# Kernel tuning notes

Measured on AMD Instinct MI355X. Metric: run time of the kernel, lower is better.

The kernel has to match this reference:

```python
import jax, jax.numpy as jnp
import numpy as np

N_NODES = 50000
N_EDGES = 800000
D = 128
NEG_SLOPE = 0.01
LN_EPS = 1e-5


def gcn_conv(x, W, b, src, dst, n_nodes):
    # Linear transform: [N, D_in] @ [D_in, D_out]
    h = x @ W
    # Symmetric degree normalization (self-loops already included in src/dst)
    deg = jax.ops.segment_sum(jnp.ones_like(dst, dtype=h.dtype), dst, num_segments=n_nodes)
    dinv = jnp.where(deg > 0, jax.lax.rsqrt(deg), 0.0)
    coef = dinv[src] * dinv[dst]                      # [E]
    msg = h[src] * coef[:, None]                      # gather + scale, [E, D]
    out = jax.ops.segment_sum(msg, dst, num_segments=n_nodes)  # scatter-add
    return out + b


def layer_norm(x, gamma, beta):
    mu = jnp.mean(x, axis=-1, keepdims=True)
    var = jnp.mean(jnp.square(x - mu), axis=-1, keepdims=True)
    return (x - mu) * jax.lax.rsqrt(var + LN_EPS) * gamma + beta


def setup_inputs() -> dict:
    key = jax.random.key(0)
    ks = jax.random.split(key, 8)
    x = jax.random.normal(ks[0], (N_NODES, D), dtype=jnp.float32)
    edge_index = jax.random.randint(ks[1], (2, N_EDGES), 0, N_NODES, dtype=jnp.int64)
    s = 1.0 / np.sqrt(D)
    W1 = jax.random.uniform(ks[2], (D, D), jnp.float32, -s, s)
    b1 = jnp.zeros((D,), jnp.float32)
    W2 = jax.random.uniform(ks[3], (D, D), jnp.float32, -s, s)
    b2 = jnp.zeros((D,), jnp.float32)
    ln1_g = jnp.ones((D,), jnp.float32)
    ln1_b = jnp.zeros((D,), jnp.float32)
    ln2_g = jnp.ones((D,), jnp.float32)
    ln2_b = jnp.zeros((D,), jnp.float32)
    return {"x": x, "edge_index": edge_index, "W1": W1, "b1": b1,
            "ln1_g": ln1_g, "ln1_b": ln1_b, "W2": W2, "b2": b2,
            "ln2_g": ln2_g, "ln2_b": ln2_b}


def reference(x, edge_index, W1, b1, ln1_g, ln1_b, W2, b2, ln2_g, ln2_b):
    n = x.shape[0]
    # add self-loops (PyG GCNConv default)
    loops = jnp.arange(n, dtype=edge_index.dtype)
    src = jnp.concatenate([edge_index[0], loops])
    dst = jnp.concatenate([edge_index[1], loops])

    residual = x
    h = gcn_conv(x, W1, b1, src, dst, n)
    h = jax.nn.leaky_relu(h, NEG_SLOPE)
    h = layer_norm(h + residual, ln1_g, ln1_b)
    h = gcn_conv(h, W2, b2, src, dst, n)
    return jax.nn.leaky_relu(layer_norm(h + residual, ln2_g, ln2_b), NEG_SLOPE)
```

## Files before the change

### kernel.cpp

```cpp
#include <hip/hip_runtime.h>
#include <hip/hip_bf16.h>

#define NN 50000
#define NE 800000
#define D 128
#define NEG_SLOPE 0.01f
#define LN_EPS 1e-5f

#define NPB 256
#define NB 196
#define CAP 6144
#define ECH 8192
#define NCH ((NE + ECH - 1) / ECH)
#define NDEG 256
#define NGEMM ((NN + 63) / 64)

typedef __attribute__((ext_vector_type(8))) short bf16x8;
typedef __attribute__((ext_vector_type(4))) float f32x4;
typedef __attribute__((ext_vector_type(4))) int i32x4;

__device__ inline unsigned short f2bf(float f) {
    unsigned u = __float_as_uint(f);
    unsigned r = 0x7FFFu + ((u >> 16) & 1u);
    return (unsigned short)((u + r) >> 16);
}
__device__ inline void bf2x(unsigned u, float& lo, float& hi) {
    lo = __uint_as_float(u << 16);
    hi = __uint_as_float(u & 0xFFFF0000u);
}


struct BucketLDS {
    int hist[NB], lcur[NB], gbase[NB];
    int tmp[256];
};
struct GemmLDS {
    unsigned short a[64 * 128];
};
union FusedLDS { BucketLDS b; GemmLDS g; };

__device__ inline void gemm_body(GemmLDS& L, const float* __restrict__ A,
                                 const unsigned short* __restrict__ WT,
                                 unsigned short* __restrict__ out, int m0, int n, int t) {
    #pragma unroll
    for (int it = 0; it < 4; ++it) {
        int idx = it * 256 + t;
        int row = idx >> 4, c = idx & 15;
        int grow = m0 + row;
        uint4 w = make_uint4(0u, 0u, 0u, 0u);
        if (grow < n) {
            float4 v0 = *(const float4*)&A[(size_t)grow * D + c * 8];
            float4 v1 = *(const float4*)&A[(size_t)grow * D + c * 8 + 4];
            w.x = (unsigned)f2bf(v0.x) | ((unsigned)f2bf(v0.y) << 16);
            w.y = (unsigned)f2bf(v0.z) | ((unsigned)f2bf(v0.w) << 16);
            w.z = (unsigned)f2bf(v1.x) | ((unsigned)f2bf(v1.y) << 16);
            w.w = (unsigned)f2bf(v1.z) | ((unsigned)f2bf(v1.w) << 16);
        }
        int byte = (row * 256 + c * 16) ^ ((row & 7) << 4);
        *(uint4*)((char*)L.a + byte) = w;
    }
    __syncthreads();

    int wv = t >> 6, l = t & 63;
    int lrow = l & 15, lgrp = l >> 4;
    int arow = wv * 16 + lrow;

    f32x4 acc[8];
    #pragma unroll
    for (int nf = 0; nf < 8; ++nf) acc[nf] = (f32x4){0.f, 0.f, 0.f, 0.f};

    #pragma unroll
    for (int kk = 0; kk < 4; ++kk) {
        int abyte = (arow * 256 + kk * 64 + lgrp * 16) ^ ((arow & 7) << 4);
        bf16x8 afrag = *(bf16x8*)((char*)L.a + abyte);
        #pragma unroll
        for (int nf = 0; nf < 8; ++nf) {
            int bcol = nf * 16 + lrow;
            bf16x8 bfrag = *(const bf16x8*)&WT[bcol * 128 + kk * 32 + lgrp * 8];
            acc[nf] = __builtin_amdgcn_mfma_f32_16x16x32_bf16(afrag, bfrag, acc[nf], 0, 0, 0);
        }
    }

    #pragma unroll
    for (int nf = 0; nf < 8; ++nf) {
        #pragma unroll
        for (int r = 0; r < 4; ++r) {
            int grow = m0 + wv * 16 + lgrp * 4 + r;
            if (grow < n) out[(size_t)grow * D + nf * 16 + lrow] = f2bf(acc[nf][r]);
        }
    }
}

__global__ __launch_bounds__(256) void fused1(const int* __restrict__ src,
                                              const int* __restrict__ dst,
                                              int* __restrict__ bcursor,
                                              int2* __restrict__ bedge,
                                              int* __restrict__ deg,
                                              const float* __restrict__ x,
                                              const unsigned short* __restrict__ wt1,
                                              unsigned short* __restrict__ hbf) {
    __shared__ FusedLDS u;
    int bid = blockIdx.x, t = threadIdx.x;

    if (bid < NCH) {
        BucketLDS& L = u.b;
        int e0 = bid * ECH;
        int ecnt = min(ECH, NE - e0);
        if (t < NB) L.hist[t] = 0;
        __syncthreads();
        for (int k = t; k < ecnt; k += 256) atomicAdd(&L.hist[dst[e0 + k] >> 8], 1);
        __syncthreads();
        if (t < NB) {
            L.gbase[t] = atomicAdd(&bcursor[t], L.hist[t]);
            L.lcur[t] = 0;
        }
        __syncthreads();
        for (int k = t; k < ecnt; k += 256) {
            int s = src[e0 + k], d = dst[e0 + k];
            int b = d >> 8;
            int p = atomicAdd(&L.lcur[b], 1);
            bedge[(size_t)b * CAP + L.gbase[b] + p] = make_int2(s, d);
        }
    } else if (bid < NCH + NDEG) {
        for (int k = (bid - NCH) * 256 + t; k < NE; k += NDEG * 256)
            atomicAdd(&deg[dst[k]], 1);
    } else {
        gemm_body(u.g, x, wt1, hbf, (bid - NCH - NDEG) * 64, NN, t);
    }
}

__global__ __launch_bounds__(256) void fused2(const int2* __restrict__ bedge,
                                              const int* __restrict__ bcnt,
                                              const int* __restrict__ deg,
                                              float* __restrict__ dinv,
                                              int2* __restrict__ rowinfo,
                                              int* __restrict__ ticket,
                                              int2* __restrict__ csr_pair) {
    __shared__ int tmp[256];
    __shared__ int rl[NPB], cur[NPB];
    __shared__ float sdinv[NPB];
    __shared__ int base;
    int b = blockIdx.x, t = threadIdx.x;
    int node = b * NPB + t;
    int dg = (node < NN) ? deg[node] : 0;
    float dv = rsqrtf((float)(dg + 1));
    sdinv[t] = dv;
    int pdeg = (dg + 7) & ~7;
    tmp[t] = pdeg;
    __syncthreads();
    for (int off = 1; off < 256; off <<= 1) {
        int uu = (t >= off) ? tmp[t - off] : 0;
        __syncthreads();
        tmp[t] += uu;
        __syncthreads();
    }
    if (t == 255) base = atomicAdd(ticket, tmp[255]);
    __syncthreads();
    int start = base + tmp[t] - pdeg;
    rl[t] = start;
    cur[t] = 0;
    if (node < NN) {
        dinv[node] = dv;
        rowinfo[node] = make_int2(start, pdeg);
    }
    __syncthreads();
    int s0 = b * CAP, s1 = s0 + bcnt[b];
    for (int k = s0 + t; k < s1; k += 256) {
        int2 eg = bedge[k];
        int li = eg.y & 255;
        int p = atomicAdd(&cur[li], 1);
        int ds = deg[eg.x];
        float coef = rsqrtf((float)(ds + 1)) * sdinv[li];
        csr_pair[rl[li] + p] = make_int2(eg.x, __float_as_int(coef));
    }
    __syncthreads();
    int dgc = cur[t];
    int pend = (dgc + 7) & ~7;
    int selfsrc = (node < NN) ? node : 0;
    for (int k = dgc; k < pend; ++k)
        csr_pair[rl[t] + k] = make_int2(selfsrc, 0);
}

__global__ void wt_pack2(const float* __restrict__ W1, const float* __restrict__ W2,
                         unsigned short* __restrict__ WT1, unsigned short* __restrict__ WT2) {
    int tid = blockIdx.x * 256 + threadIdx.x;
    const float* W = (tid < D * D) ? W1 : W2;
    unsigned short* WT = (tid < D * D) ? WT1 : WT2;
    int id = tid & (D * D - 1);
    int nn = id & 127, k = id >> 7;
    WT[nn * 128 + k] = f2bf(W[k * 128 + nn]);
}


__device__ inline void agg8(const unsigned* __restrict__ h, const int2* __restrict__ csr_pair,
                            int e, int lane, float& accx, float& accy) {
    i32x4 q0 = __builtin_nontemporal_load((const i32x4*)(csr_pair + e + 0));
    i32x4 q1 = __builtin_nontemporal_load((const i32x4*)(csr_pair + e + 2));
    i32x4 q2 = __builtin_nontemporal_load((const i32x4*)(csr_pair + e + 4));
    i32x4 q3 = __builtin_nontemporal_load((const i32x4*)(csr_pair + e + 6));
    unsigned g0 = h[(size_t)q0[0] * (D / 2) + lane];
    unsigned g1 = h[(size_t)q0[2] * (D / 2) + lane];
    unsigned g2 = h[(size_t)q1[0] * (D / 2) + lane];
    unsigned g3 = h[(size_t)q1[2] * (D / 2) + lane];
    unsigned g4 = h[(size_t)q2[0] * (D / 2) + lane];
    unsigned g5 = h[(size_t)q2[2] * (D / 2) + lane];
    unsigned g6 = h[(size_t)q3[0] * (D / 2) + lane];
    unsigned g7 = h[(size_t)q3[2] * (D / 2) + lane];
    float ax, ay, c;
    c = __int_as_float(q0[1]); bf2x(g0, ax, ay); accx = fmaf(c, ax, accx); accy = fmaf(c, ay, accy);
    c = __int_as_float(q0[3]); bf2x(g1, ax, ay); accx = fmaf(c, ax, accx); accy = fmaf(c, ay, accy);
    c = __int_as_float(q1[1]); bf2x(g2, ax, ay); accx = fmaf(c, ax, accx); accy = fmaf(c, ay, accy);
    c = __int_as_float(q1[3]); bf2x(g3, ax, ay); accx = fmaf(c, ax, accx); accy = fmaf(c, ay, accy);
    c = __int_as_float(q2[1]); bf2x(g4, ax, ay); accx = fmaf(c, ax, accx); accy = fmaf(c, ay, accy);
    c = __int_as_float(q2[3]); bf2x(g5, ax, ay); accx = fmaf(c, ax, accx); accy = fmaf(c, ay, accy);
    c = __int_as_float(q3[1]); bf2x(g6, ax, ay); accx = fmaf(c, ax, accx); accy = fmaf(c, ay, accy);
    c = __int_as_float(q3[3]); bf2x(g7, ax, ay); accx = fmaf(c, ax, accx); accy = fmaf(c, ay, accy);
}

__device__ inline void agg_2node(const unsigned* __restrict__ h,
                                 const int2* __restrict__ csr_pair,
                                 int eA, int eA1, int eB, int eB1, int lane,
                                 float& aAx, float& aAy, float& aBx, float& aBy) {
    while (eA < eA1 && eB < eB1) {
        i32x4 qA0 = __builtin_nontemporal_load((const i32x4*)(csr_pair + eA + 0));
        i32x4 qA1 = __builtin_nontemporal_load((const i32x4*)(csr_pair + eA + 2));
        i32x4 qA2 = __builtin_nontemporal_load((const i32x4*)(csr_pair + eA + 4));
        i32x4 qA3 = __builtin_nontemporal_load((const i32x4*)(csr_pair + eA + 6));
        i32x4 qB0 = __builtin_nontemporal_load((const i32x4*)(csr_pair + eB + 0));
        i32x4 qB1 = __builtin_nontemporal_load((const i32x4*)(csr_pair + eB + 2));
        i32x4 qB2 = __builtin_nontemporal_load((const i32x4*)(csr_pair + eB + 4));
        i32x4 qB3 = __builtin_nontemporal_load((const i32x4*)(csr_pair + eB + 6));
        unsigned gA0 = h[(size_t)qA0[0] * (D / 2) + lane];
        unsigned gA1 = h[(size_t)qA0[2] * (D / 2) + lane];
        unsigned gA2 = h[(size_t)qA1[0] * (D / 2) + lane];
        unsigned gA3 = h[(size_t)qA1[2] * (D / 2) + lane];
        unsigned gA4 = h[(size_t)qA2[0] * (D / 2) + lane];
        unsigned gA5 = h[(size_t)qA2[2] * (D / 2) + lane];
        unsigned gA6 = h[(size_t)qA3[0] * (D / 2) + lane];
        unsigned gA7 = h[(size_t)qA3[2] * (D / 2) + lane];
        unsigned gB0 = h[(size_t)qB0[0] * (D / 2) + lane];
        unsigned gB1 = h[(size_t)qB0[2] * (D / 2) + lane];
        unsigned gB2 = h[(size_t)qB1[0] * (D / 2) + lane];
        unsigned gB3 = h[(size_t)qB1[2] * (D / 2) + lane];
        unsigned gB4 = h[(size_t)qB2[0] * (D / 2) + lane];
        unsigned gB5 = h[(size_t)qB2[2] * (D / 2) + lane];
        unsigned gB6 = h[(size_t)qB3[0] * (D / 2) + lane];
        unsigned gB7 = h[(size_t)qB3[2] * (D / 2) + lane];
        float ax, ay, c;
        c = __int_as_float(qA0[1]); bf2x(gA0, ax, ay); aAx = fmaf(c, ax, aAx); aAy = fmaf(c, ay, aAy);
        c = __int_as_float(qA0[3]); bf2x(gA1, ax, ay); aAx = fmaf(c, ax, aAx); aAy = fmaf(c, ay, aAy);
        c = __int_as_float(qA1[1]); bf2x(gA2, ax, ay); aAx = fmaf(c, ax, aAx); aAy = fmaf(c, ay, aAy);
        c = __int_as_float(qA1[3]); bf2x(gA3, ax, ay); aAx = fmaf(c, ax, aAx); aAy = fmaf(c, ay, aAy);
        c = __int_as_float(qA2[1]); bf2x(gA4, ax, ay); aAx = fmaf(c, ax, aAx); aAy = fmaf(c, ay, aAy);
        c = __int_as_float(qA2[3]); bf2x(gA5, ax, ay); aAx = fmaf(c, ax, aAx); aAy = fmaf(c, ay, aAy);
        c = __int_as_float(qA3[1]); bf2x(gA6, ax, ay); aAx = fmaf(c, ax, aAx); aAy = fmaf(c, ay, aAy);
        c = __int_as_float(qA3[3]); bf2x(gA7, ax, ay); aAx = fmaf(c, ax, aAx); aAy = fmaf(c, ay, aAy);
        c = __int_as_float(qB0[1]); bf2x(gB0, ax, ay); aBx = fmaf(c, ax, aBx); aBy = fmaf(c, ay, aBy);
        c = __int_as_float(qB0[3]); bf2x(gB1, ax, ay); aBx = fmaf(c, ax, aBx); aBy = fmaf(c, ay, aBy);
        c = __int_as_float(qB1[1]); bf2x(gB2, ax, ay); aBx = fmaf(c, ax, aBx); aBy = fmaf(c, ay, aBy);
        c = __int_as_float(qB1[3]); bf2x(gB3, ax, ay); aBx = fmaf(c, ax, aBx); aBy = fmaf(c, ay, aBy);
        c = __int_as_float(qB2[1]); bf2x(gB4, ax, ay); aBx = fmaf(c, ax, aBx); aBy = fmaf(c, ay, aBy);
        c = __int_as_float(qB2[3]); bf2x(gB5, ax, ay); aBx = fmaf(c, ax, aBx); aBy = fmaf(c, ay, aBy);
        c = __int_as_float(qB3[1]); bf2x(gB6, ax, ay); aBx = fmaf(c, ax, aBx); aBy = fmaf(c, ay, aBy);
        c = __int_as_float(qB3[3]); bf2x(gB7, ax, ay); aBx = fmaf(c, ax, aBx); aBy = fmaf(c, ay, aBy);
        eA += 8; eB += 8;
    }
    while (eA < eA1) { agg8(h, csr_pair, eA, lane, aAx, aAy); eA += 8; }
    while (eB < eB1) { agg8(h, csr_pair, eB, lane, aBx, aBy); eB += 8; }
}

__global__ __launch_bounds__(512) void agg_ln1_gemm(const unsigned* __restrict__ h,
                                                    const float* __restrict__ x,
                                                    const float* __restrict__ bias,
                                                    const float* __restrict__ gamma,
                                                    const float* __restrict__ beta,
                                                    const float* __restrict__ dinv,
                                                    const int2* __restrict__ rowinfo,
                                                    const int2* __restrict__ csr_pair,
                                                    const unsigned short* __restrict__ wt2,
                                                    unsigned short* __restrict__ hbf2) {
    __shared__ __align__(16) unsigned short w_lds[128 * 128];
    __shared__ __align__(16) unsigned short a_lds[16 * 128];
    int t = threadIdx.x;

    #pragma unroll
    for (int it = 0; it < 4; ++it) {
        int idx = it * 512 + t;
        int row = idx >> 4, c = idx & 15;
        uint4 v = *(const uint4*)&wt2[row * 128 + c * 8];
        int byte = (row * 256 + c * 16) ^ ((row & 7) << 4);
        *(uint4*)((char*)w_lds + byte) = v;
    }

    int wid = t >> 6, lane = t & 63;
    int iA = blockIdx.x * 16 + wid * 2;
    int iB = iA + 1;
    float diA = dinv[iA], diB = dinv[iB];

    float hx, hy;
    bf2x(h[(size_t)iA * (D / 2) + lane], hx, hy);
    float aAx = diA * diA * hx, aAy = diA * diA * hy;
    bf2x(h[(size_t)iB * (D / 2) + lane], hx, hy);
    float aBx = diB * diB * hx, aBy = diB * diB * hy;

    int2 riA = rowinfo[iA];
    int2 riB = rowinfo[iB];
    int eA = __builtin_amdgcn_readfirstlane(riA.x);
    int eA1 = eA + __builtin_amdgcn_readfirstlane(riA.y);
    int eB = __builtin_amdgcn_readfirstlane(riB.x);
    int eB1 = eB + __builtin_amdgcn_readfirstlane(riB.y);
    agg_2node(h, csr_pair, eA, eA1, eB, eB1, lane, aAx, aAy, aBx, aBy);

    float2 bv = *(const float2*)&bias[2 * lane];
    float2 gv = *(const float2*)&gamma[2 * lane];
    float2 bt = *(const float2*)&beta[2 * lane];

    aAx += bv.x; aAy += bv.y;
    aBx += bv.x; aBy += bv.y;
    aAx = aAx > 0.f ? aAx : NEG_SLOPE * aAx;
    aAy = aAy > 0.f ? aAy : NEG_SLOPE * aAy;
    aBx = aBx > 0.f ? aBx : NEG_SLOPE * aBx;
    aBy = aBy > 0.f ? aBy : NEG_SLOPE * aBy;

    size_t rowA = (size_t)iA * D + 2 * lane;
    size_t rowB = (size_t)iB * D + 2 * lane;
    float2 xA = *(const float2*)&x[rowA];
    float2 xB = *(const float2*)&x[rowB];
    float vA0 = aAx + xA.x, vA1 = aAy + xA.y;
    float vB0 = aBx + xB.x, vB1 = aBy + xB.y;

    float sA1 = vA0 + vA1, sA2 = vA0 * vA0 + vA1 * vA1;
    float sB1 = vB0 + vB1, sB2 = vB0 * vB0 + vB1 * vB1;
    #pragma unroll
    for (int off = 1; off < 64; off <<= 1) {
        sA1 += __shfl_xor(sA1, off, 64);
        sA2 += __shfl_xor(sA2, off, 64);
        sB1 += __shfl_xor(sB1, off, 64);
        sB2 += __shfl_xor(sB2, off, 64);
    }
    float muA = sA1 * (1.f / 128.f);
    float varA = fmaxf(sA2 * (1.f / 128.f) - muA * muA, 0.f);
    float rsA = rsqrtf(varA + LN_EPS);
    float muB = sB1 * (1.f / 128.f);
    float varB = fmaxf(sB2 * (1.f / 128.f) - muB * muB, 0.f);
    float rsB = rsqrtf(varB + LN_EPS);

    float oA0 = (vA0 - muA) * rsA * gv.x + bt.x;
    float oA1 = (vA1 - muA) * rsA * gv.y + bt.y;
    float oB0 = (vB0 - muB) * rsB * gv.x + bt.x;
    float oB1 = (vB1 - muB) * rsB * gv.y + bt.y;

    int rA = wid * 2, rB = wid * 2 + 1;
    unsigned dwA = (unsigned)f2bf(oA0) | ((unsigned)f2bf(oA1) << 16);
    unsigned dwB = (unsigned)f2bf(oB0) | ((unsigned)f2bf(oB1) << 16);
    int byteA = (rA * 256 + lane * 4) ^ ((rA & 7) << 4);
    int byteB = (rB * 256 + lane * 4) ^ ((rB & 7) << 4);
    *(unsigned*)((char*)a_lds + byteA) = dwA;
    *(unsigned*)((char*)a_lds + byteB) = dwB;
    __syncthreads();

    int lrow = lane & 15, lgrp = lane >> 4;
    f32x4 acc = (f32x4){0.f, 0.f, 0.f, 0.f};
    #pragma unroll
    for (int kk = 0; kk < 4; ++kk) {
        int abyte = (lrow * 256 + kk * 64 + lgrp * 16) ^ ((lrow & 7) << 4);
        bf16x8 afrag = *(bf16x8*)((char*)a_lds + abyte);
        int bcol = wid * 16 + lrow;
        int bbyte = (bcol * 256 + kk * 64 + lgrp * 16) ^ ((bcol & 7) << 4);
        bf16x8 bfrag = *(bf16x8*)((char*)w_lds + bbyte);
        acc = __builtin_amdgcn_mfma_f32_16x16x32_bf16(afrag, bfrag, acc, 0, 0, 0);
    }
    #pragma unroll
    for (int r = 0; r < 4; ++r) {
        int grow = blockIdx.x * 16 + lgrp * 4 + r;
        hbf2[(size_t)grow * D + wid * 16 + lrow] = f2bf(acc[r]);
    }
}

__global__ __launch_bounds__(256) void agg_ln2(const unsigned* __restrict__ h,
                                               const float* __restrict__ x,
                                               const float* __restrict__ bias,
                                               const float* __restrict__ gamma,
                                               const float* __restrict__ beta,
                                               const float* __restrict__ dinv,
                                               const int2* __restrict__ rowinfo,
                                               const int2* __restrict__ csr_pair,
                                               float* __restrict__ out) {
    int wid = threadIdx.x >> 6;
    int lane = threadIdx.x & 63;
    int iA = blockIdx.x * 8 + wid * 2;
    int iB = iA + 1;
    float diA = dinv[iA], diB = dinv[iB];

    float hx, hy;
    bf2x(h[(size_t)iA * (D / 2) + lane], hx, hy);
    float aAx = diA * diA * hx, aAy = diA * diA * hy;
    bf2x(h[(size_t)iB * (D / 2) + lane], hx, hy);
    float aBx = diB * diB * hx, aBy = diB * diB * hy;

    int2 riA = rowinfo[iA];
    int2 riB = rowinfo[iB];
    int eA = __builtin_amdgcn_readfirstlane(riA.x);
    int eA1 = eA + __builtin_amdgcn_readfirstlane(riA.y);
    int eB = __builtin_amdgcn_readfirstlane(riB.x);
    int eB1 = eB + __builtin_amdgcn_readfirstlane(riB.y);
    agg_2node(h, csr_pair, eA, eA1, eB, eB1, lane, aAx, aAy, aBx, aBy);

    float2 bv = *(const float2*)&bias[2 * lane];
    float2 gv = *(const float2*)&gamma[2 * lane];
    float2 bt = *(const float2*)&beta[2 * lane];

    aAx += bv.x; aAy += bv.y;
    aBx += bv.x; aBy += bv.y;
    size_t rowA = (size_t)iA * D + 2 * lane;
    size_t rowB = (size_t)iB * D + 2 * lane;
    float2 xA = *(const float2*)&x[rowA];
    float2 xB = *(const float2*)&x[rowB];
    float vA0 = aAx + xA.x, vA1 = aAy + xA.y;
    float vB0 = aBx + xB.x, vB1 = aBy + xB.y;

    float sA1 = vA0 + vA1, sA2 = vA0 * vA0 + vA1 * vA1;
    float sB1 = vB0 + vB1, sB2 = vB0 * vB0 + vB1 * vB1;
    #pragma unroll
    for (int off = 1; off < 64; off <<= 1) {
        sA1 += __shfl_xor(sA1, off, 64);
        sA2 += __shfl_xor(sA2, off, 64);
        sB1 += __shfl_xor(sB1, off, 64);
        sB2 += __shfl_xor(sB2, off, 64);
    }
    float muA = sA1 * (1.f / 128.f);
    float varA = fmaxf(sA2 * (1.f / 128.f) - muA * muA, 0.f);
    float rsA = rsqrtf(varA + LN_EPS);
    float muB = sB1 * (1.f / 128.f);
    float varB = fmaxf(sB2 * (1.f / 128.f) - muB * muB, 0.f);
    float rsB = rsqrtf(varB + LN_EPS);

    float oA0 = (vA0 - muA) * rsA * gv.x + bt.x;
    float oA1 = (vA1 - muA) * rsA * gv.y + bt.y;
    float oB0 = (vB0 - muB) * rsB * gv.x + bt.x;
    float oB1 = (vB1 - muB) * rsB * gv.y + bt.y;
    oA0 = oA0 > 0.f ? oA0 : NEG_SLOPE * oA0;
    oA1 = oA1 > 0.f ? oA1 : NEG_SLOPE * oA1;
    oB0 = oB0 > 0.f ? oB0 : NEG_SLOPE * oB0;
    oB1 = oB1 > 0.f ? oB1 : NEG_SLOPE * oB1;
    *(float2*)&out[rowA] = make_float2(oA0, oA1);
    *(float2*)&out[rowB] = make_float2(oB0, oB1);
}

extern "C" void kernel_launch(void* const* d_in, const int* in_sizes, int n_in,
                              void* d_out, int out_size, void* d_ws, size_t ws_size,
                              hipStream_t stream) {
    const float* x    = (const float*)d_in[0];
    const int*   ei   = (const int*)d_in[1];
    const float* W1   = (const float*)d_in[2];
    const float* b1   = (const float*)d_in[3];
    const float* ln1g = (const float*)d_in[4];
    const float* ln1b = (const float*)d_in[5];
    const float* W2   = (const float*)d_in[6];
    const float* b2   = (const float*)d_in[7];
    const float* ln2g = (const float*)d_in[8];
    const float* ln2b = (const float*)d_in[9];
    float* out = (float*)d_out;

    const int* srcp = ei;
    const int* dstp = ei + NE;

    char* ws = (char*)d_ws;
    size_t p = 0;
    auto alloc = [&](size_t bytes) {
        char* r = ws + p;
        p += (bytes + 255) & ~(size_t)255;
        return r;
    };
    int*   deg      = (int*)alloc(NN * 4);
    int*   bcursor  = (int*)alloc((NB + 1) * 4);
    int2*  rowinfo  = (int2*)alloc((size_t)NN * 8);
    float* dinv     = (float*)alloc(NN * 4);
    int2*  bedge    = (int2*)alloc((size_t)NB * CAP * 8);
    int2*  csr_pair = (int2*)alloc(((size_t)NE + 8 * NN) * 8);
    unsigned short* hbf  = (unsigned short*)alloc((size_t)NN * D * 2);
    unsigned short* hbf2 = (unsigned short*)alloc((size_t)NN * D * 2);
    unsigned short* wt1  = (unsigned short*)alloc(D * D * 2);
    unsigned short* wt2  = (unsigned short*)alloc(D * D * 2);

    size_t zbytes = (char*)rowinfo - (char*)deg;
    hipMemsetAsync(deg, 0, zbytes, stream);

    wt_pack2<<<2 * D * D / 256, 256, 0, stream>>>(W1, W2, wt1, wt2);

    fused1<<<NCH + NDEG + NGEMM, 256, 0, stream>>>(srcp, dstp, bcursor, bedge, deg,
                                                   x, wt1, hbf);

    fused2<<<NB, 256, 0, stream>>>(bedge, bcursor, deg, dinv, rowinfo,
                                   &bcursor[NB], csr_pair);

    agg_ln1_gemm<<<NN / 16, 512, 0, stream>>>((const unsigned*)hbf, x, b1, ln1g, ln1b,
                                              dinv, rowinfo, csr_pair, wt2, hbf2);

    agg_ln2<<<NN / 8, 256, 0, stream>>>((const unsigned*)hbf2, x, b2, ln2g, ln2b,
                                        dinv, rowinfo, csr_pair, out);
}
```

Baseline: 149.8 us.

## Split fused preprocessing kernels; compute degrees from buckets; stage weights in LDS

Splits the fused bucket/degree/GEMM kernel into separate kernels. Node degrees are now counted per bucket in LDS, which removes the global atomic degree pass and its memset. The degree/prefix-sum step and the CSR scatter become two kernels, with coefficients read from a precomputed dinv array. The GEMM now stages the transposed weights in swizzled LDS instead of reading them from global memory. The cost is extra kernel launches and the loss of overlap between the GEMM and the bucketing work.

```diff
diff --git a/kernel.cpp b/kernel.cpp
--- a/kernel.cpp
+++ b/kernel.cpp
@@ -12,8 +12,6 @@
 #define CAP 6144
 #define ECH 8192
 #define NCH ((NE + ECH - 1) / ECH)
-#define NDEG 256
-#define NGEMM ((NN + 63) / 64)
 
 typedef __attribute__((ext_vector_type(8))) short bf16x8;
 typedef __attribute__((ext_vector_type(4))) float f32x4;
@@ -30,18 +28,120 @@
 }
 
 
-struct BucketLDS {
-    int hist[NB], lcur[NB], gbase[NB];
-    int tmp[256];
-};
-struct GemmLDS {
-    unsigned short a[64 * 128];
-};
-union FusedLDS { BucketLDS b; GemmLDS g; };
-
-__device__ inline void gemm_body(GemmLDS& L, const float* __restrict__ A,
-                                 const unsigned short* __restrict__ WT,
-                                 unsigned short* __restrict__ out, int m0, int n, int t) {
+__global__ __launch_bounds__(256) void bucket_scatter(const int* __restrict__ src,
+                                                      const int* __restrict__ dst,
+                                                      int* __restrict__ bcursor,
+                                                      int2* __restrict__ bedge) {
+    __shared__ int hist[NB], lcur[NB], gbase[NB];
+    int t = threadIdx.x;
+    int e0 = blockIdx.x * ECH;
+    int ecnt = min(ECH, NE - e0);
+    if (t < NB) hist[t] = 0;
+    __syncthreads();
+    for (int k = t; k < ecnt; k += 256) atomicAdd(&hist[dst[e0 + k] >> 8], 1);
+    __syncthreads();
+    if (t < NB) {
+        gbase[t] = atomicAdd(&bcursor[t], hist[t]);
+        lcur[t] = 0;
+    }
+    __syncthreads();
+    for (int k = t; k < ecnt; k += 256) {
+        int s = src[e0 + k], d = dst[e0 + k];
+        int b = d >> 8;
+        int p = atomicAdd(&lcur[b], 1);
+        bedge[(size_t)b * CAP + gbase[b] + p] = make_int2(s, d);
+    }
+}
+
+__global__ __launch_bounds__(256) void node_count(const int2* __restrict__ bedge,
+                                                  const int* __restrict__ bcnt,
+                                                  float* __restrict__ dinv,
+                                                  int2* __restrict__ rowinfo,
+                                                  int* __restrict__ ticket) {
+    __shared__ int h[NPB];
+    __shared__ int tmp[256];
+    __shared__ int base;
+    int b = blockIdx.x, t = threadIdx.x;
+    h[t] = 0;
+    __syncthreads();
+    int s0 = b * CAP, s1 = s0 + bcnt[b];
+    for (int k = s0 + t; k < s1; k += 256) atomicAdd(&h[bedge[k].y & 255], 1);
+    __syncthreads();
+    int deg = h[t];
+    int node = b * NPB + t;
+    int pdeg = (deg + 7) & ~7;
+    tmp[t] = pdeg;
+    __syncthreads();
+    for (int off = 1; off < 256; off <<= 1) {
+        int uu = (t >= off) ? tmp[t - off] : 0;
+        __syncthreads();
+        tmp[t] += uu;
+        __syncthreads();
+    }
+    if (t == 255) base = atomicAdd(ticket, tmp[255]);
+    __syncthreads();
+    if (node < NN) {
+        dinv[node] = rsqrtf((float)(deg + 1));
+        rowinfo[node] = make_int2(base + tmp[t] - pdeg, pdeg);
+    }
+}
+
+__global__ __launch_bounds__(256) void csr_scatter(const int2* __restrict__ bedge,
+                                                   const int* __restrict__ bcnt,
+                                                   const int2* __restrict__ rowinfo,
+                                                   const float* __restrict__ dinv,
+                                                   int2* __restrict__ csr_pair) {
+    __shared__ int cur[NPB];
+    __shared__ int rl[NPB];
+    __shared__ float sdinv[NPB];
+    int b = blockIdx.x, t = threadIdx.x;
+    int node = b * NPB + t;
+    rl[t] = (node < NN) ? rowinfo[node].x : 0;
+    sdinv[t] = (node < NN) ? dinv[node] : 0.f;
+    cur[t] = 0;
+    __syncthreads();
+    int s0 = b * CAP, s1 = s0 + bcnt[b];
+    for (int k = s0 + t; k < s1; k += 256) {
+        int2 eg = bedge[k];
+        int li = eg.y & 255;
+        int p = atomicAdd(&cur[li], 1);
+        float coef = dinv[eg.x] * sdinv[li];
+        csr_pair[rl[li] + p] = make_int2(eg.x, __float_as_int(coef));
+    }
+    __syncthreads();
+    int dgc = cur[t];
+    int pend = (dgc + 7) & ~7;
+    int selfsrc = (node < NN) ? node : 0;
+    for (int k = dgc; k < pend; ++k)
+        csr_pair[rl[t] + k] = make_int2(selfsrc, 0);
+}
+
+__global__ void wt_pack2(const float* __restrict__ W1, const float* __restrict__ W2,
+                         unsigned short* __restrict__ WT1, unsigned short* __restrict__ WT2) {
+    int tid = blockIdx.x * 256 + threadIdx.x;
+    const float* W = (tid < D * D) ? W1 : W2;
+    unsigned short* WT = (tid < D * D) ? WT1 : WT2;
+    int id = tid & (D * D - 1);
+    int nn = id & 127, k = id >> 7;
+    WT[nn * 128 + k] = f2bf(W[k * 128 + nn]);
+}
+
+__global__ __launch_bounds__(256) void gemm_mfma(const float* __restrict__ A,
+                                                 const unsigned short* __restrict__ WT,
+                                                 unsigned short* __restrict__ out, int n) {
+    __shared__ __align__(16) unsigned short a_lds[64 * 128];
+    __shared__ __align__(16) unsigned short w_lds[128 * 128];
+    int t = threadIdx.x;
+    int m0 = blockIdx.x * 64;
+
+    #pragma unroll
+    for (int it = 0; it < 8; ++it) {
+        int idx = it * 256 + t;
+        int row = idx >> 4, c = idx & 15;
+        uint4 v = *(const uint4*)&WT[row * 128 + c * 8];
+        int byte = (row * 256 + c * 16) ^ ((row & 7) << 4);
+        *(uint4*)((char*)w_lds + byte) = v;
+    }
     #pragma unroll
     for (int it = 0; it < 4; ++it) {
         int idx = it * 256 + t;
@@ -57,7 +157,7 @@
             w.w = (unsigned)f2bf(v1.z) | ((unsigned)f2bf(v1.w) << 16);
         }
         int byte = (row * 256 + c * 16) ^ ((row & 7) << 4);
-        *(uint4*)((char*)L.a + byte) = w;
+        *(uint4*)((char*)a_lds + byte) = w;
     }
     __syncthreads();
 
@@ -72,11 +172,12 @@
     #pragma unroll
     for (int kk = 0; kk < 4; ++kk) {
         int abyte = (arow * 256 + kk * 64 + lgrp * 16) ^ ((arow & 7) << 4);
-        bf16x8 afrag = *(bf16x8*)((char*)L.a + abyte);
+        bf16x8 afrag = *(bf16x8*)((char*)a_lds + abyte);
         #pragma unroll
         for (int nf = 0; nf < 8; ++nf) {
             int bcol = nf * 16 + lrow;
-            bf16x8 bfrag = *(const bf16x8*)&WT[bcol * 128 + kk * 32 + lgrp * 8];
+            int bbyte = (bcol * 256 + kk * 64 + lgrp * 16) ^ ((bcol & 7) << 4);
+            bf16x8 bfrag = *(bf16x8*)((char*)w_lds + bbyte);
             acc[nf] = __builtin_amdgcn_mfma_f32_16x16x32_bf16(afrag, bfrag, acc[nf], 0, 0, 0);
         }
     }
@@ -89,106 +190,6 @@
             if (grow < n) out[(size_t)grow * D + nf * 16 + lrow] = f2bf(acc[nf][r]);
         }
     }
-}
-
-__global__ __launch_bounds__(256) void fused1(const int* __restrict__ src,
-                                              const int* __restrict__ dst,
-                                              int* __restrict__ bcursor,
-                                              int2* __restrict__ bedge,
-                                              int* __restrict__ deg,
-                                              const float* __restrict__ x,
-                                              const unsigned short* __restrict__ wt1,
-                                              unsigned short* __restrict__ hbf) {
-    __shared__ FusedLDS u;
-    int bid = blockIdx.x, t = threadIdx.x;
-
-    if (bid < NCH) {
-        BucketLDS& L = u.b;
-        int e0 = bid * ECH;
-        int ecnt = min(ECH, NE - e0);
-        if (t < NB) L.hist[t] = 0;
-        __syncthreads();
-        for (int k = t; k < ecnt; k += 256) atomicAdd(&L.hist[dst[e0 + k] >> 8], 1);
-        __syncthreads();
-        if (t < NB) {
-            L.gbase[t] = atomicAdd(&bcursor[t], L.hist[t]);
-            L.lcur[t] = 0;
-        }
-        __syncthreads();
-        for (int k = t; k < ecnt; k += 256) {
-            int s = src[e0 + k], d = dst[e0 + k];
-            int b = d >> 8;
-            int p = atomicAdd(&L.lcur[b], 1);
-            bedge[(size_t)b * CAP + L.gbase[b] + p] = make_int2(s, d);
-        }
-    } else if (bid < NCH + NDEG) {
-        for (int k = (bid - NCH) * 256 + t; k < NE; k += NDEG * 256)
-            atomicAdd(&deg[dst[k]], 1);
-    } else {
-        gemm_body(u.g, x, wt1, hbf, (bid - NCH - NDEG) * 64, NN, t);
-    }
-}
-
-__global__ __launch_bounds__(256) void fused2(const int2* __restrict__ bedge,
-                                              const int* __restrict__ bcnt,
-                                              const int* __restrict__ deg,
-                                              float* __restrict__ dinv,
-                                              int2* __restrict__ rowinfo,
-                                              int* __restrict__ ticket,
-                                              int2* __restrict__ csr_pair) {
-    __shared__ int tmp[256];
-    __shared__ int rl[NPB], cur[NPB];
-    __shared__ float sdinv[NPB];
-    __shared__ int base;
-    int b = blockIdx.x, t = threadIdx.x;
-    int node = b * NPB + t;
-    int dg = (node < NN) ? deg[node] : 0;
-    float dv = rsqrtf((float)(dg + 1));
-    sdinv[t] = dv;
-    int pdeg = (dg + 7) & ~7;
-    tmp[t] = pdeg;
-    __syncthreads();
-    for (int off = 1; off < 256; off <<= 1) {
-        int uu = (t >= off) ? tmp[t - off] : 0;
-        __syncthreads();
-        tmp[t] += uu;
-        __syncthreads();
-    }
-    if (t == 255) base = atomicAdd(ticket, tmp[255]);
-    __syncthreads();
-    int start = base + tmp[t] - pdeg;
-    rl[t] = start;
-    cur[t] = 0;
-    if (node < NN) {
-        dinv[node] = dv;
-        rowinfo[node] = make_int2(start, pdeg);
-    }
-    __syncthreads();
-    int s0 = b * CAP, s1 = s0 + bcnt[b];
-    for (int k = s0 + t; k < s1; k += 256) {
-        int2 eg = bedge[k];
-        int li = eg.y & 255;
-        int p = atomicAdd(&cur[li], 1);
-        int ds = deg[eg.x];
-        float coef = rsqrtf((float)(ds + 1)) * sdinv[li];
-        csr_pair[rl[li] + p] = make_int2(eg.x, __float_as_int(coef));
-    }
-    __syncthreads();
-    int dgc = cur[t];
-    int pend = (dgc + 7) & ~7;
-    int selfsrc = (node < NN) ? node : 0;
-    for (int k = dgc; k < pend; ++k)
-        csr_pair[rl[t] + k] = make_int2(selfsrc, 0);
-}
-
-__global__ void wt_pack2(const float* __restrict__ W1, const float* __restrict__ W2,
-                         unsigned short* __restrict__ WT1, unsigned short* __restrict__ WT2) {
-    int tid = blockIdx.x * 256 + threadIdx.x;
-    const float* W = (tid < D * D) ? W1 : W2;
-    unsigned short* WT = (tid < D * D) ? WT1 : WT2;
-    int id = tid & (D * D - 1);
-    int nn = id & 127, k = id >> 7;
-    WT[nn * 128 + k] = f2bf(W[k * 128 + nn]);
 }
 
 
@@ -472,7 +473,6 @@
         p += (bytes + 255) & ~(size_t)255;
         return r;
     };
-    int*   deg      = (int*)alloc(NN * 4);
     int*   bcursor  = (int*)alloc((NB + 1) * 4);
     int2*  rowinfo  = (int2*)alloc((size_t)NN * 8);
     float* dinv     = (float*)alloc(NN * 4);
@@ -483,16 +483,14 @@
     unsigned short* wt1  = (unsigned short*)alloc(D * D * 2);
     unsigned short* wt2  = (unsigned short*)alloc(D * D * 2);
 
-    size_t zbytes = (char*)rowinfo - (char*)deg;
-    hipMemsetAsync(deg, 0, zbytes, stream);
+    hipMemsetAsync(bcursor, 0, (NB + 1) * 4, stream);
 
     wt_pack2<<<2 * D * D / 256, 256, 0, stream>>>(W1, W2, wt1, wt2);
 
-    fused1<<<NCH + NDEG + NGEMM, 256, 0, stream>>>(srcp, dstp, bcursor, bedge, deg,
-                                                   x, wt1, hbf);
-
-    fused2<<<NB, 256, 0, stream>>>(bedge, bcursor, deg, dinv, rowinfo,
-                                   &bcursor[NB], csr_pair);
+    bucket_scatter<<<NCH, 256, 0, stream>>>(srcp, dstp, bcursor, bedge);
+    gemm_mfma<<<(NN + 63) / 64, 256, 0, stream>>>(x, wt1, hbf, NN);
+    node_count<<<NB, 256, 0, stream>>>(bedge, bcursor, dinv, rowinfo, &bcursor[NB]);
+    csr_scatter<<<NB, 256, 0, stream>>>(bedge, bcursor, rowinfo, dinv, csr_pair);
 
     agg_ln1_gemm<<<NN / 16, 512, 0, stream>>>((const unsigned*)hbf, x, b1, ln1g, ln1b,
                                               dinv, rowinfo, csr_pair, wt2, hbf2);
```

New measurement: 133.7 us. 10.7% less time.
